# Kernel optimization log

Measured on AMD Instinct MI355X. Metric: run time of the kernel, lower is better.

The kernel has to match this reference:

```python
import jax, jax.numpy as jnp
import numpy as np

B, S, I, H, O = 512, 1024, 1, 2048, 128


def _uniform(k, shape, bound):
    return jax.random.uniform(k, shape, jnp.float32, -bound, bound)


def setup_inputs() -> dict:
    key = jax.random.key(0)
    ks = jax.random.split(key, 12)
    gate_bound = 1.0 / np.sqrt(I + H)  # torch nn.Linear default init range
    out_bound = 1.0 / np.sqrt(H)
    return {
        "x": jax.random.normal(ks[0], (B, S, I), jnp.float32),
        "Wg": _uniform(ks[1], (H, I + H), gate_bound),
        "bg": _uniform(ks[2], (H,), gate_bound),
        "Wi": _uniform(ks[3], (H, I + H), gate_bound),
        "bi": _uniform(ks[4], (H,), gate_bound),
        "Wf": _uniform(ks[5], (H, I + H), gate_bound),
        "bf": _uniform(ks[6], (H,), gate_bound),
        "Wo": _uniform(ks[7], (H, I + H), gate_bound),
        "bo": _uniform(ks[8], (H,), gate_bound),
        "Wy": _uniform(ks[9], (O, H), out_bound),
        "by": _uniform(ks[10], (O,), out_bound),
    }


def reference(x, Wg, bg, Wi, bi, Wf, bf, Wo, bo, Wy, by):
    # Batched, scan-over-time LSTM: same math as the original nested Python
    # loops (zero initial h/c, 4 separate gate Linears on concat([x_t, h]),
    # c = g*i + c*f, h = tanh(c)*o, output Linear on the last h).
    b_, h_dim = x.shape[0], Wg.shape[0]
    # Stack the 4 gate weights -> single fused matmul per step. [4H, I+H]
    W = jnp.concatenate([Wg, Wi, Wf, Wo], axis=0)
    b = jnp.concatenate([bg, bi, bf, bo], axis=0)
    h0 = jnp.zeros((b_, h_dim), x.dtype)
    c0 = jnp.zeros((b_, h_dim), x.dtype)

    def step(carry, xt):
        h, c = carry
        xh = jnp.concatenate([xt, h], axis=-1)  # [B, I+H]
        z = xh @ W.T + b                         # [B, 4H]
        g, i, f, o = jnp.split(z, 4, axis=-1)
        g = jnp.tanh(g)
        i = jax.nn.sigmoid(i)
        f = jax.nn.sigmoid(f)
        o = jax.nn.sigmoid(o)
        c = g * i + c * f
        h = jnp.tanh(c) * o
        return (h, c), None

    xs = jnp.swapaxes(x, 0, 1)  # [S, B, I] time-major for scan
    (h_last, _), _ = jax.lax.scan(step, (h0, c0), xs)
    return h_last @ Wy.T + by  # [B, O]
```

## Files before the change

### kernel.cpp

```cpp
#include <hip/hip_runtime.h>

typedef _Float16 f16;
typedef _Float16 f16x8 __attribute__((ext_vector_type(8)));
typedef float f32x4 __attribute__((ext_vector_type(4)));

static constexpr int kS = 1024;

static constexpr size_t OFF_WP = 0;
static constexpr size_t OFF_WX = 33554432;
static constexpr size_t OFF_BB = OFF_WX + 32768;
static constexpr size_t OFF_XT = OFF_BB + 32768;
static constexpr size_t OFF_HA = OFF_XT + 2097152;
static constexpr size_t OFF_HB = OFF_HA + 2097152;
static constexpr size_t OFF_CB = OFF_HB + 2097152;

__device__ __forceinline__ void gload16(const void* g, void* l) {
  __builtin_amdgcn_global_load_lds(
      (const __attribute__((address_space(1))) unsigned int*)g,
      (__attribute__((address_space(3))) unsigned int*)l, 16, 0, 0);
}

__device__ __forceinline__ float sigf(float x) { return 1.f / (1.f + __expf(-x)); }
__device__ __forceinline__ float tanh_fast(float x) {
  float e = __expf(2.f * x);
  return 1.f - 2.f / (e + 1.f);
}

__global__ void pack_weights(const float* __restrict__ Wg, const float* __restrict__ Wi,
                             const float* __restrict__ Wf, const float* __restrict__ Wo,
                             const float* __restrict__ bg, const float* __restrict__ bi,
                             const float* __restrict__ bf, const float* __restrict__ bo,
                             f16* __restrict__ Wp, float* __restrict__ wx, float* __restrict__ bb)
{
  const int R = blockIdx.x;
  const int p = R >> 8, r = R & 255;
  const int u = (p << 6) + (r >> 2), gsel = r & 3;
  const float* Wsrc = (gsel == 0) ? Wg : (gsel == 1) ? Wi : (gsel == 2) ? Wf : Wo;
  const float* bsrc = (gsel == 0) ? bg : (gsel == 1) ? bi : (gsel == 2) ? bf : bo;
  const float* src = Wsrc + (size_t)u * 2049;
  const int k = threadIdx.x * 8;
#pragma unroll
  for (int j = 0; j < 8; ++j)
    Wp[(size_t)R * 2048 + k + j] = (f16)src[1 + k + j];
  if (threadIdx.x == 0) { wx[R] = src[0]; bb[R] = bsrc[u]; }
}

__global__ void transpose_x(const float* __restrict__ x, float* __restrict__ xT) {
  const int idx = blockIdx.x * 256 + threadIdx.x;
  const int b = idx >> 10, t = idx & 1023;
  xT[t * 512 + b] = x[idx];
}

__global__ void zero_h(f16* hA) {
  const int idx = blockIdx.x * 256 + threadIdx.x;
  ((uint4*)hA)[idx] = make_uint4(0u, 0u, 0u, 0u);
}

__global__ __launch_bounds__(256, 1) void lstm_step(
    const f16* __restrict__ Wp, const float* __restrict__ wx,
    const float* __restrict__ bb, const float* __restrict__ xT,
    const f16* __restrict__ hin, f16* __restrict__ hout,
    float* __restrict__ cbuf, int t)
{
  extern __shared__ __align__(16) char smem[];
  f16* ldsA = (f16*)smem;
  f16* ldsB = (f16*)(smem + 65536);
  f16* ldsH = (f16*)smem;

  const int blk = blockIdx.x;
  const int p  = (blk & 7) + 8 * (blk >> 6);
  const int bp = (blk >> 3) & 7;
  const int u0 = p * 64, b0 = bp * 64;

  const int tid = threadIdx.x;
  const int w = tid >> 6, l = tid & 63;
  const int l15 = l & 15, hi = l >> 4;
  const int r3 = l >> 3, c7 = l & 7;
  const int ksw = (c7 ^ r3) * 8;

  float wxr[4][4], br[4][4];
#pragma unroll
  for (int ni = 0; ni < 4; ++ni)
#pragma unroll
    for (int r = 0; r < 4; ++r) {
      const int R = p * 256 + w * 64 + ni * 16 + hi * 4 + r;
      wxr[ni][r] = wx[R];
      br[ni][r] = bb[R];
    }

  float xv[4];
#pragma unroll
  for (int bj = 0; bj < 4; ++bj)
    xv[bj] = xT[t * 512 + b0 + bj * 16 + l15];

  float* cme = cbuf + ((size_t)blk * 256 + tid) * 16;
  float cst[4][4];
  if (t == 0) {
#pragma unroll
    for (int ni = 0; ni < 4; ++ni)
#pragma unroll
      for (int bj = 0; bj < 4; ++bj) cst[ni][bj] = 0.f;
  } else {
#pragma unroll
    for (int ni = 0; ni < 4; ++ni) {
      const float4 cv = *(const float4*)(cme + ni * 4);
      cst[ni][0] = cv.x; cst[ni][1] = cv.y; cst[ni][2] = cv.z; cst[ni][3] = cv.w;
    }
  }

  auto stage = [&](int ch) {
    const int buf = ch & 1;
    const int k0 = ch * 64;
#pragma unroll
    for (int j = 0; j < 8; ++j) {
      const int row = w * 64 + j * 8 + r3;
      gload16(Wp + (size_t)(p * 256 + row) * 2048 + (k0 + ksw),
              ldsA + buf * 16384 + (w * 64 + j * 8) * 64);
    }
#pragma unroll
    for (int j = 0; j < 2; ++j) {
      const int rb = w * 16 + j * 8 + r3;
      gload16(hin + (size_t)(b0 + rb) * 2048 + (k0 + ksw),
              ldsB + buf * 4096 + (w * 16 + j * 8) * 64);
    }
  };

  stage(0);
  __syncthreads();

  f32x4 acc[4][4];
#pragma unroll
  for (int ni = 0; ni < 4; ++ni) {
    f32x4 v;
    v[0] = br[ni][0]; v[1] = br[ni][1]; v[2] = br[ni][2]; v[3] = br[ni][3];
#pragma unroll
    for (int bj = 0; bj < 4; ++bj) acc[ni][bj] = v;
  }

#pragma unroll 2
  for (int ch = 0; ch < 32; ++ch) {
    if (ch < 31) stage(ch + 1);
    const f16* A  = ldsA + (ch & 1) * 16384;
    const f16* Bm = ldsB + (ch & 1) * 4096;
#pragma unroll
    for (int ks = 0; ks < 2; ++ks) {
      const int sw = ((ks * 4 + hi) ^ c7) * 8;
      f16x8 af[4], bf4[4];
#pragma unroll
      for (int ni = 0; ni < 4; ++ni)
        af[ni] = *(const f16x8*)(A + (w * 64 + ni * 16 + l15) * 64 + sw);
#pragma unroll
      for (int bj = 0; bj < 4; ++bj)
        bf4[bj] = *(const f16x8*)(Bm + (bj * 16 + l15) * 64 + sw);
#pragma unroll
      for (int ni = 0; ni < 4; ++ni)
#pragma unroll
        for (int bj = 0; bj < 4; ++bj)
          acc[ni][bj] = __builtin_amdgcn_mfma_f32_16x16x32_f16(af[ni], bf4[bj], acc[ni][bj], 0, 0, 0);
    }
    __syncthreads();
  }

#pragma unroll
  for (int ni = 0; ni < 4; ++ni) {
    float cnew[4];
#pragma unroll
    for (int bj = 0; bj < 4; ++bj) {
      const f32x4 a = acc[ni][bj];
      const float z0 = a[0] + xv[bj] * wxr[ni][0];
      const float z1 = a[1] + xv[bj] * wxr[ni][1];
      const float z2 = a[2] + xv[bj] * wxr[ni][2];
      const float z3 = a[3] + xv[bj] * wxr[ni][3];
      const float gg = tanh_fast(z0);
      const float ig = sigf(z1);
      const float fg = sigf(z2);
      const float og = sigf(z3);
      const float cc = gg * ig + cst[ni][bj] * fg;
      cnew[bj] = cc;
      const float hh = tanh_fast(cc) * og;
      ldsH[(bj * 16 + l15) * 72 + (w * 16 + ni * 4 + hi)] = (f16)hh;
    }
    *(float4*)(cme + ni * 4) = make_float4(cnew[0], cnew[1], cnew[2], cnew[3]);
  }
  __syncthreads();

#pragma unroll
  for (int j = 0; j < 2; ++j) {
    const int q = tid + j * 256;
    const int row = q >> 3, uc = q & 7;
    const f16x8 v = *(const f16x8*)(ldsH + row * 72 + uc * 8);
    *(f16x8*)(hout + (size_t)(b0 + row) * 2048 + u0 + uc * 8) = v;
  }
}

__global__ void out_proj(const f16* __restrict__ h, const float* __restrict__ Wy,
                         const float* __restrict__ by, float* __restrict__ y)
{
  const int gi = blockIdx.x * 256 + threadIdx.x;
  const int o = gi & 127, b = gi >> 7;
  const f16* hr = h + (size_t)b * 2048;
  const float* wr = Wy + (size_t)o * 2048;
  float acc = 0.f;
  for (int k = 0; k < 2048; k += 8) {
    const f16x8 hv = *(const f16x8*)(hr + k);
    const float4 wa = *(const float4*)(wr + k);
    const float4 wb = *(const float4*)(wr + k + 4);
    acc += (float)hv[0] * wa.x + (float)hv[1] * wa.y + (float)hv[2] * wa.z + (float)hv[3] * wa.w
         + (float)hv[4] * wb.x + (float)hv[5] * wb.y + (float)hv[6] * wb.z + (float)hv[7] * wb.w;
  }
  y[gi] = acc + by[o];
}

extern "C" void kernel_launch(void* const* d_in, const int* in_sizes, int n_in,
                              void* d_out, int out_size, void* d_ws, size_t ws_size,
                              hipStream_t stream)
{
  const float* x  = (const float*)d_in[0];
  const float* Wg = (const float*)d_in[1];
  const float* bg = (const float*)d_in[2];
  const float* Wi = (const float*)d_in[3];
  const float* bi = (const float*)d_in[4];
  const float* Wf = (const float*)d_in[5];
  const float* bf = (const float*)d_in[6];
  const float* Wo = (const float*)d_in[7];
  const float* bo = (const float*)d_in[8];
  const float* Wy = (const float*)d_in[9];
  const float* by = (const float*)d_in[10];
  float* y = (float*)d_out;

  char* ws = (char*)d_ws;
  f16*   Wp = (f16*)(ws + OFF_WP);
  float* wx = (float*)(ws + OFF_WX);
  float* bb = (float*)(ws + OFF_BB);
  float* xT = (float*)(ws + OFF_XT);
  f16*   hA = (f16*)(ws + OFF_HA);
  f16*   hB = (f16*)(ws + OFF_HB);
  float* cb = (float*)(ws + OFF_CB);

  pack_weights<<<8192, 256, 0, stream>>>(Wg, Wi, Wf, Wo, bg, bi, bf, bo, Wp, wx, bb);
  transpose_x<<<2048, 256, 0, stream>>>(x, xT);
  zero_h<<<512, 256, 0, stream>>>(hA);

  (void)hipFuncSetAttribute((const void*)lstm_step,
                            hipFuncAttributeMaxDynamicSharedMemorySize, 131072);
  for (int t = 0; t < kS; ++t) {
    const f16* hin = (t & 1) ? hB : hA;
    f16*      hout = (t & 1) ? hA : hB;
    lstm_step<<<256, 256, 81920, stream>>>(Wp, wx, bb, xT, hin, hout, cb, t);
  }

  out_proj<<<256, 256, 0, stream>>>(hA, Wy, by, y);
}
```

Measured before the change: 30.66 ms.

## Retile LSTM step to 128x128 blocks with triple-buffered async LDS pipeline

Result: no change. 30.26 ms (-1.3%).

```diff
diff --git a/kernel.cpp b/kernel.cpp
--- a/kernel.cpp
+++ b/kernel.cpp
@@ -64,16 +64,17 @@
 {
   extern __shared__ __align__(16) char smem[];
   f16* ldsA = (f16*)smem;
-  f16* ldsB = (f16*)(smem + 65536);
+  f16* ldsB = (f16*)(smem + 49152);
   f16* ldsH = (f16*)smem;
 
   const int blk = blockIdx.x;
-  const int p  = (blk & 7) + 8 * (blk >> 6);
-  const int bp = (blk >> 3) & 7;
-  const int u0 = p * 64, b0 = bp * 64;
+  const int p  = (blk & 7) + 8 * (blk >> 5);
+  const int bp = (blk >> 3) & 3;
+  const int u0 = p * 32, b0 = bp * 128;
 
   const int tid = threadIdx.x;
   const int w = tid >> 6, l = tid & 63;
+  const int wr = w >> 1, wc = w & 1;
   const int l15 = l & 15, hi = l >> 4;
   const int r3 = l >> 3, c7 = l & 7;
   const int ksw = (c7 ^ r3) * 8;
@@ -83,7 +84,7 @@
   for (int ni = 0; ni < 4; ++ni)
 #pragma unroll
     for (int r = 0; r < 4; ++r) {
-      const int R = p * 256 + w * 64 + ni * 16 + hi * 4 + r;
+      const int R = p * 128 + wr * 64 + ni * 16 + hi * 4 + r;
       wxr[ni][r] = wx[R];
       br[ni][r] = bb[R];
     }
@@ -91,7 +92,7 @@
   float xv[4];
 #pragma unroll
   for (int bj = 0; bj < 4; ++bj)
-    xv[bj] = xT[t * 512 + b0 + bj * 16 + l15];
+    xv[bj] = xT[t * 512 + b0 + wc * 64 + bj * 16 + l15];
 
   float* cme = cbuf + ((size_t)blk * 256 + tid) * 16;
   float cst[4][4];
@@ -103,30 +104,26 @@
   } else {
 #pragma unroll
     for (int ni = 0; ni < 4; ++ni) {
-      const float4 cv = *(const float4*)(cme + ni * 4);
-      cst[ni][0] = cv.x; cst[ni][1] = cv.y; cst[ni][2] = cv.z; cst[ni][3] = cv.w;
-    }
-  }
-
-  auto stage = [&](int ch) {
-    const int buf = ch & 1;
-    const int k0 = ch * 64;
-#pragma unroll
-    for (int j = 0; j < 8; ++j) {
-      const int row = w * 64 + j * 8 + r3;
-      gload16(Wp + (size_t)(p * 256 + row) * 2048 + (k0 + ksw),
-              ldsA + buf * 16384 + (w * 64 + j * 8) * 64);
-    }
-#pragma unroll
-    for (int j = 0; j < 2; ++j) {
-      const int rb = w * 16 + j * 8 + r3;
-      gload16(hin + (size_t)(b0 + rb) * 2048 + (k0 + ksw),
-              ldsB + buf * 4096 + (w * 16 + j * 8) * 64);
+      const f32x4 cv = __builtin_nontemporal_load((const f32x4*)(cme + ni * 4));
+      cst[ni][0] = cv[0]; cst[ni][1] = cv[1]; cst[ni][2] = cv[2]; cst[ni][3] = cv[3];
+    }
+  }
+
+  auto stage = [&](int ch, int buf) {
+    const size_t kof = (size_t)ch * 64 + ksw;
+#pragma unroll
+    for (int j = 0; j < 4; ++j) {
+      const int row = w * 32 + j * 8;
+      gload16(Wp + (size_t)(p * 128 + row + r3) * 2048 + kof,
+              ldsA + buf * 8192 + row * 64);
+    }
+#pragma unroll
+    for (int j = 0; j < 4; ++j) {
+      const int row = w * 32 + j * 8;
+      gload16(hin + (size_t)(b0 + row + r3) * 2048 + kof,
+              ldsB + buf * 8192 + row * 64);
     }
   };
-
-  stage(0);
-  __syncthreads();
 
   f32x4 acc[4][4];
 #pragma unroll
@@ -137,33 +134,52 @@
     for (int bj = 0; bj < 4; ++bj) acc[ni][bj] = v;
   }
 
-#pragma unroll 2
+  stage(0, 0);
+  stage(1, 1);
+
+  int bufc = 0;
+#pragma unroll 1
   for (int ch = 0; ch < 32; ++ch) {
-    if (ch < 31) stage(ch + 1);
-    const f16* A  = ldsA + (ch & 1) * 16384;
-    const f16* Bm = ldsB + (ch & 1) * 4096;
+    if (ch < 30) {
+      int bufs = bufc - 1; if (bufs < 0) bufs = 2;
+      stage(ch + 2, bufs);
+      asm volatile("s_waitcnt vmcnt(16)" ::: "memory");
+    } else if (ch == 30) {
+      asm volatile("s_waitcnt vmcnt(8)" ::: "memory");
+    } else {
+      asm volatile("s_waitcnt vmcnt(0)" ::: "memory");
+    }
+    __builtin_amdgcn_sched_barrier(0);
+    __builtin_amdgcn_s_barrier();
+    __builtin_amdgcn_sched_barrier(0);
+
+    const f16* A  = ldsA + bufc * 8192;
+    const f16* Bm = ldsB + bufc * 8192;
 #pragma unroll
     for (int ks = 0; ks < 2; ++ks) {
       const int sw = ((ks * 4 + hi) ^ c7) * 8;
-      f16x8 af[4], bf4[4];
+      f16x8 af[4], bfr[4];
 #pragma unroll
       for (int ni = 0; ni < 4; ++ni)
-        af[ni] = *(const f16x8*)(A + (w * 64 + ni * 16 + l15) * 64 + sw);
+        af[ni] = *(const f16x8*)(A + (wr * 64 + ni * 16 + l15) * 64 + sw);
 #pragma unroll
       for (int bj = 0; bj < 4; ++bj)
-        bf4[bj] = *(const f16x8*)(Bm + (bj * 16 + l15) * 64 + sw);
+        bfr[bj] = *(const f16x8*)(Bm + (wc * 64 + bj * 16 + l15) * 64 + sw);
 #pragma unroll
       for (int ni = 0; ni < 4; ++ni)
 #pragma unroll
         for (int bj = 0; bj < 4; ++bj)
-          acc[ni][bj] = __builtin_amdgcn_mfma_f32_16x16x32_f16(af[ni], bf4[bj], acc[ni][bj], 0, 0, 0);
-    }
-    __syncthreads();
+          acc[ni][bj] = __builtin_amdgcn_mfma_f32_16x16x32_f16(af[ni], bfr[bj], acc[ni][bj], 0, 0, 0);
+    }
+
+    __builtin_amdgcn_sched_barrier(0);
+    __builtin_amdgcn_s_barrier();
+    bufc = (bufc == 2) ? 0 : bufc + 1;
   }
 
 #pragma unroll
   for (int ni = 0; ni < 4; ++ni) {
-    float cnew[4];
+    f32x4 cnew;
 #pragma unroll
     for (int bj = 0; bj < 4; ++bj) {
       const f32x4 a = acc[ni][bj];
@@ -178,18 +194,18 @@
       const float cc = gg * ig + cst[ni][bj] * fg;
       cnew[bj] = cc;
       const float hh = tanh_fast(cc) * og;
-      ldsH[(bj * 16 + l15) * 72 + (w * 16 + ni * 4 + hi)] = (f16)hh;
-    }
-    *(float4*)(cme + ni * 4) = make_float4(cnew[0], cnew[1], cnew[2], cnew[3]);
+      ldsH[(wc * 64 + bj * 16 + l15) * 40 + (wr * 16 + ni * 4 + hi)] = (f16)hh;
+    }
+    __builtin_nontemporal_store(cnew, (f32x4*)(cme + ni * 4));
   }
   __syncthreads();
 
 #pragma unroll
   for (int j = 0; j < 2; ++j) {
     const int q = tid + j * 256;
-    const int row = q >> 3, uc = q & 7;
-    const f16x8 v = *(const f16x8*)(ldsH + row * 72 + uc * 8);
-    *(f16x8*)(hout + (size_t)(b0 + row) * 2048 + u0 + uc * 8) = v;
+    const int row = q >> 2, uc = q & 3;
+    const f16x8 v = *(const f16x8*)(ldsH + row * 40 + uc * 8);
+    __builtin_nontemporal_store(v, (f16x8*)(hout + (size_t)(b0 + row) * 2048 + u0 + uc * 8));
   }
 }
 
@@ -246,7 +262,7 @@
   for (int t = 0; t < kS; ++t) {
     const f16* hin = (t & 1) ? hB : hA;
     f16*      hout = (t & 1) ? hA : hB;
-    lstm_step<<<256, 256, 81920, stream>>>(Wp, wx, bb, xT, hin, hout, cb, t);
+    lstm_step<<<256, 256, 98304, stream>>>(Wp, wx, bb, xT, hin, hout, cb, t);
   }
 
   out_proj<<<256, 256, 0, stream>>>(hA, Wy, by, y);
```
